# Performance work log

Measured on AMD Instinct MI355X. Metric: run time of the kernel, lower is better.

The kernel has to match this reference:

```python
import jax, jax.numpy as jnp
import numpy as np

WINDOW_LENGTH = 512
ORDER = 26


def hann_window(n):
    # periodic Hann (matches torch.hann_window default)
    i = jnp.arange(n, dtype=jnp.float32)
    return 0.5 * (1.0 - jnp.cos(2.0 * jnp.pi * i / n))


def upsample_linear(g, hop):
    # F.interpolate(mode='linear', align_corners=False), scale_factor=hop
    B, F = g.shape
    j = jnp.arange(F * hop, dtype=jnp.float32)
    src = jnp.clip((j + 0.5) / hop - 0.5, 0.0, F - 1.0)
    i0 = jnp.floor(src).astype(jnp.int32)
    i1 = jnp.minimum(i0 + 1, F - 1)
    w = src - i0.astype(jnp.float32)
    return g[:, i0] * (1.0 - w) + g[:, i1] * w


def lpc_synthesis_batch(x, a):
    # all-pole IIR: y[n] = x[n] - sum_k a[k] * y[n-1-k]; x [N,W], a [N,order]
    N, W = x.shape
    order = a.shape[1]

    def step(carry, xt):  # carry [N,order] newest-first, xt [N]
        yt = xt - jnp.sum(a * carry, axis=1)
        carry = jnp.concatenate([yt[:, None], carry[:, :-1]], axis=1)
        return carry, yt

    _, y = jax.lax.scan(step, jnp.zeros((N, order), x.dtype), x.T)
    return y.T  # [N, W]


def setup_inputs() -> dict:
    key = jax.random.key(0)
    k1, k2, k3 = jax.random.split(key, 3)
    B, T, F = 32, 128000, 1000
    ex = jax.random.normal(k1, (B, T), dtype=jnp.float32)
    gain = jax.random.uniform(k2, (B, F), dtype=jnp.float32)
    # small coefficients keep the all-pole filter stable
    a = jax.random.normal(k3, (B, F, ORDER), dtype=jnp.float32) * 0.05
    window = hann_window(WINDOW_LENGTH)
    return {"ex": ex, "gain": gain, "a": a, "window": window, "hop_length": 128}


def reference(ex, gain, a, window, hop_length):
    W = window.shape[0]
    pad = (W - hop_length) // 2
    B = ex.shape[0]
    ug = upsample_linear(gain, hop_length)  # [B, F*hop]
    T = min(ex.shape[1], ug.shape[1])
    exg = ex[:, :T] * ug[:, :T]
    exp = jnp.pad(exg, ((0, 0), (pad, pad)))
    nframes = (exp.shape[1] - W) // hop_length + 1
    idx = jnp.arange(nframes)[:, None] * hop_length + jnp.arange(W)[None, :]  # [F,W]
    unfolded = exp[:, idx]  # [B, F, W]
    a_ = a[:, :nframes].reshape(-1, a.shape[-1])
    filt = lpc_synthesis_batch(unfolded.reshape(-1, W), a_).reshape(B, nframes, W)
    windowed = filt * window  # window applied per in-frame sample (diag kernel)
    L = (nframes - 1) * hop_length + W
    flat_idx = idx.reshape(-1)
    ola = jnp.zeros((B, L), filt.dtype).at[:, flat_idx].add(windowed.reshape(B, -1))
    norm = jnp.zeros((L,), filt.dtype).at[flat_idx].add(jnp.tile(window, nframes))
    return ola[:, pad:L - pad] / norm[pad:L - pad]
```

## Files before the change

kernel.cpp:

```cpp
#include <hip/hip_runtime.h>
#include <hip/hip_bf16.h>

#define BATCH   32
#define TLEN    128000
#define FGAIN   1000
#define ORDER   26
#define WLEN    512
#define HOP     128
#define PAD     192
#define TPAD    (TLEN + 2*PAD)
#define NFRAME  1000
#define NTOT    (BATCH*NFRAME)

#define CHUNK   64
#define NCHUNK  ((NFRAME + CHUNK - 1) / CHUNK)
#define XS_SPAN (CHUNK*HOP + WLEN - HOP)
#define XS_LDS  8656
#define GS_LDS  80
#define YSTRIDE 53

__global__ __launch_bounds__(64) void k_lpc(const float* __restrict__ ex,
                                            const float* __restrict__ gain,
                                            const float* __restrict__ acoef,
                                            float* __restrict__ fw) {
  __shared__ float xs[XS_LDS];
  __shared__ float gs[GS_LDS];
  __shared__ float ys[CHUNK * YSTRIDE];

  const int lane = threadIdx.x;
  const int n0   = blockIdx.x * CHUNK;
  const int b    = blockIdx.y;
  const float* __restrict__ exr = ex + (size_t)b * TLEN;
  const float* __restrict__ gr  = gain + b * FGAIN;

  const int GBASE = n0 - 2;
  for (int i = lane; i < 72; i += 64) {
    int gidx = GBASE + i;
    gidx = gidx < 0 ? 0 : (gidx > FGAIN - 1 ? FGAIN - 1 : gidx);
    gs[i] = gr[gidx];
  }
  __syncthreads();

  for (int i = lane; i < XS_SPAN / 4; i += 64) {
    int s = 4 * i;
    int j = n0 * HOP + s - PAD;
    float vv[4] = {0.f, 0.f, 0.f, 0.f};
    if (j >= 0 && j < TLEN) {
      float4 e = *reinterpret_cast<const float4*>(exr + j);
      float ee[4] = {e.x, e.y, e.z, e.w};
#pragma unroll
      for (int c = 0; c < 4; ++c) {
        float src = ((float)(j + c) + 0.5f) * (1.0f / (float)HOP) - 0.5f;
        src = fminf(fmaxf(src, 0.0f), (float)(FGAIN - 1));
        int   i0 = (int)src;
        float w  = src - (float)i0;
        int   i1 = i0 + 1; if (i1 > FGAIN - 1) i1 = FGAIN - 1;
        float g  = gs[i0 - GBASE] * (1.0f - w) + gs[i1 - GBASE] * w;
        vv[c] = ee[c] * g;
      }
    }
    int base = s + (s >> 7);
    xs[base + 0] = vv[0];  xs[base + 1] = vv[1];
    xs[base + 2] = vv[2];  xs[base + 3] = vv[3];
  }
  __syncthreads();

  int f = b * NFRAME + n0 + lane;
  int f_cl = f < NTOT ? f : NTOT - 1;
  const float* __restrict__ ap = acoef + (size_t)f_cl * ORDER;
  const size_t fwrow0 = (size_t)(b * NFRAME + n0) * WLEN;

  float a[ORDER], h[ORDER];
#pragma unroll
  for (int q = 0; q < 13; ++q) {
    float2 v = *reinterpret_cast<const float2*>(ap + 2 * q);
    a[2 * q] = v.x;  a[2 * q + 1] = v.y;
  }
#pragma unroll
  for (int k = 0; k < ORDER; ++k) h[k] = 0.0f;

  float buf[52];

#define LPC_STEP(s) {                                                      \
    float xv = buf[(s)];                                                   \
    float p0 = xv, p1 = 0.f, p2 = 0.f, p3 = 0.f;                           \
    _Pragma("unroll")                                                      \
    for (int k = 1; k < ORDER; ++k) {                                      \
      float hv = h[((s) - 1 - k + 2 * ORDER) % ORDER];                     \
      int sel = k & 3;                                                     \
      if      (sel == 0) p0 -= a[k] * hv;                                  \
      else if (sel == 1) p1 -= a[k] * hv;                                  \
      else if (sel == 2) p2 -= a[k] * hv;                                  \
      else               p3 -= a[k] * hv;                                  \
    }                                                                      \
    float rest = (p0 + p1) + (p2 + p3);                                    \
    float y = rest - a[0] * h[((s) + ORDER - 1) % ORDER];                  \
    h[(s) % ORDER] = y;                                                    \
    ys[lane * YSTRIDE + (s)] = y;                                          \
  }

#define LOAD_BUF(nq) {                                                     \
    _Pragma("unroll")                                                      \
    for (int q = 0; q < (nq); ++q) {                                       \
      int u = t + 4 * q;                                                   \
      int base = lane * 129 + u + (u >> 7);                                \
      buf[4 * q + 0] = xs[base + 0];                                       \
      buf[4 * q + 1] = xs[base + 1];                                       \
      buf[4 * q + 2] = xs[base + 2];                                       \
      buf[4 * q + 3] = xs[base + 3];                                       \
    }                                                                      \
  }

#define STORE_YS(nq) {                                                     \
    __syncthreads();                                                       \
    _Pragma("unroll")                                                      \
    for (int jj = 0; jj < 4; ++jj) {                                       \
      int q = (lane & 3) + 4 * jj;                                         \
      if (q < (nq)) {                                                      \
        _Pragma("unroll")                                                  \
        for (int rr = 0; rr < 4; ++rr) {                                   \
          int r = rr * 16 + (lane >> 2);                                   \
          if ((n0 + r) < NFRAME) {                                         \
            float4 vv = make_float4(ys[r * YSTRIDE + 4 * q + 0],           \
                                    ys[r * YSTRIDE + 4 * q + 1],           \
                                    ys[r * YSTRIDE + 4 * q + 2],           \
                                    ys[r * YSTRIDE + 4 * q + 3]);          \
            *reinterpret_cast<float4*>(fw + fwrow0 + (size_t)r * WLEN      \
                                       + t + 4 * q) = vv;                  \
          }                                                                \
        }                                                                  \
      }                                                                    \
    }                                                                      \
    __syncthreads();                                                       \
  }

  int t = 0;
  for (int sb = 0; sb < 9; ++sb) {
    LOAD_BUF(13)
#pragma unroll
    for (int s = 0; s < 52; ++s) {
      LPC_STEP(s)
    }
    STORE_YS(13)
    t += 52;
  }
  LOAD_BUF(11)
#pragma unroll
  for (int s = 0; s < 44; ++s) {
    LPC_STEP(s)
  }
  STORE_YS(11)
#undef LPC_STEP
#undef LOAD_BUF
#undef STORE_YS
}

__global__ __launch_bounds__(256) void k_ola(const float* __restrict__ fw,
                                             const float* __restrict__ win,
                                             float* __restrict__ out) {
  int gid = blockIdx.x * 256 + threadIdx.x;
  const int total4 = BATCH * TLEN / 4;
  if (gid >= total4) return;
  int idx = gid * 4;
  int b  = idx / TLEN;
  int j0 = idx - b * TLEN;
  int p0 = j0 + PAD;

  int lo = (p0 - 381) / HOP;
  if (lo < 0) lo = 0;
  int hi = p0 / HOP;
  if (hi > NFRAME - 1) hi = NFRAME - 1;

  float ax = 0.f, ay = 0.f, az = 0.f, aw = 0.f;
  float nx = 0.f, ny = 0.f, nz = 0.f, nw = 0.f;
  for (int n = lo; n <= hi; ++n) {
    int w0 = p0 - n * HOP;
    const float4 fv = *reinterpret_cast<const float4*>(fw + ((size_t)b * NFRAME + n) * WLEN + w0);
    const float4 wv = *reinterpret_cast<const float4*>(win + w0);
    ax += fv.x * wv.x;  ay += fv.y * wv.y;  az += fv.z * wv.z;  aw += fv.w * wv.w;
    nx += wv.x;         ny += wv.y;         nz += wv.z;         nw += wv.w;
  }
  float4 o = make_float4(ax / nx, ay / ny, az / nz, aw / nw);
  *reinterpret_cast<float4*>(out + idx) = o;
}

extern "C" void kernel_launch(void* const* d_in, const int* in_sizes, int n_in,
                              void* d_out, int out_size, void* d_ws, size_t ws_size,
                              hipStream_t stream) {
  const float* ex   = (const float*)d_in[0];
  const float* gain = (const float*)d_in[1];
  const float* a    = (const float*)d_in[2];
  const float* win  = (const float*)d_in[3];
  float* outp = (float*)d_out;

  float* fw = (float*)d_ws;

  {
    hipLaunchKernelGGL(k_lpc, dim3(NCHUNK, BATCH), dim3(64), 0, stream,
                       ex, gain, a, fw);
  }
  {
    int total4 = BATCH * TLEN / 4;
    int blocks = (total4 + 255) / 256;
    hipLaunchKernelGGL(k_ola, dim3(blocks), dim3(256), 0, stream, fw, win, outp);
  }
}
```

Before: 132.2 us.

## Batch global loads in staging, stage LPC coefs via LDS, use wave-level LDS fences

The excitation staging loop now issues eight float4 global loads before computing gain-interpolated values, so more memory requests are in flight per lane. The LPC coefficients for the chunk are loaded coalesced into LDS and then read per lane, replacing strided per-thread global loads. The __syncthreads around the ys transpose are replaced by s_waitcnt lgkmcnt(0), which is safe only because the block is a single 64-lane wave. The staging bound check changes from j<TLEN to j<=TLEN-4, which holds for these aligned sizes.

```diff
diff --git a/kernel.cpp b/kernel.cpp
--- a/kernel.cpp
+++ b/kernel.cpp
@@ -19,12 +19,15 @@
 #define GS_LDS  80
 #define YSTRIDE 53
 
+#define WAVE_LDS_FENCE() asm volatile("s_waitcnt lgkmcnt(0)" ::: "memory")
+
 __global__ __launch_bounds__(64) void k_lpc(const float* __restrict__ ex,
                                             const float* __restrict__ gain,
                                             const float* __restrict__ acoef,
                                             float* __restrict__ fw) {
   __shared__ float xs[XS_LDS];
   __shared__ float gs[GS_LDS];
+  __shared__ float as_lin[CHUNK * ORDER];
   __shared__ float ys[CHUNK * YSTRIDE];
 
   const int lane = threadIdx.x;
@@ -41,44 +44,88 @@
   }
   __syncthreads();
 
-  for (int i = lane; i < XS_SPAN / 4; i += 64) {
-    int s = 4 * i;
-    int j = n0 * HOP + s - PAD;
-    float vv[4] = {0.f, 0.f, 0.f, 0.f};
-    if (j >= 0 && j < TLEN) {
-      float4 e = *reinterpret_cast<const float4*>(exr + j);
-      float ee[4] = {e.x, e.y, e.z, e.w};
-#pragma unroll
-      for (int c = 0; c < 4; ++c) {
-        float src = ((float)(j + c) + 0.5f) * (1.0f / (float)HOP) - 0.5f;
-        src = fminf(fmaxf(src, 0.0f), (float)(FGAIN - 1));
-        int   i0 = (int)src;
-        float w  = src - (float)i0;
-        int   i1 = i0 + 1; if (i1 > FGAIN - 1) i1 = FGAIN - 1;
-        float g  = gs[i0 - GBASE] * (1.0f - w) + gs[i1 - GBASE] * w;
-        vv[c] = ee[c] * g;
-      }
-    }
-    int base = s + (s >> 7);
-    xs[base + 0] = vv[0];  xs[base + 1] = vv[1];
-    xs[base + 2] = vv[2];  xs[base + 3] = vv[3];
-  }
+  {
+    const int e0_4 = (b * NFRAME + n0) * ORDER / 4;
+    const int lim4 = NTOT * ORDER / 4;
+    for (int v = lane; v < CHUNK * ORDER / 4; v += 64) {
+      float4 c = make_float4(0.f, 0.f, 0.f, 0.f);
+      if (e0_4 + v < lim4)
+        c = *reinterpret_cast<const float4*>(acoef + 4 * (size_t)(e0_4 + v));
+      *reinterpret_cast<float4*>(as_lin + 4 * v) = c;
+    }
+  }
+
+  const int sbase = n0 * HOP;
+#define STAGE_COMPUTE(IDX4, EVAL) {                                        \
+    int sc_s = 4 * (IDX4);                                                 \
+    int sc_j = sbase + sc_s - PAD;                                         \
+    float sc_v[4] = {0.f, 0.f, 0.f, 0.f};                                  \
+    if (sc_j >= 0 && sc_j <= TLEN - 4) {                                   \
+      float sc_e[4] = {(EVAL).x, (EVAL).y, (EVAL).z, (EVAL).w};            \
+      _Pragma("unroll")                                                    \
+      for (int sc_c = 0; sc_c < 4; ++sc_c) {                               \
+        float sc_src = ((float)(sc_j + sc_c) + 0.5f) * (1.0f / (float)HOP) \
+                       - 0.5f;                                             \
+        sc_src = fminf(fmaxf(sc_src, 0.0f), (float)(FGAIN - 1));           \
+        int   sc_i0 = (int)sc_src;                                         \
+        float sc_w  = sc_src - (float)sc_i0;                               \
+        int   sc_i1 = sc_i0 + 1; if (sc_i1 > FGAIN - 1) sc_i1 = FGAIN - 1; \
+        float sc_g  = gs[sc_i0 - GBASE] * (1.0f - sc_w)                    \
+                    + gs[sc_i1 - GBASE] * sc_w;                            \
+        sc_v[sc_c] = sc_e[sc_c] * sc_g;                                    \
+      }                                                                    \
+    }                                                                      \
+    int sc_b = sc_s + (sc_s >> 7);              \
+    xs[sc_b + 0] = sc_v[0];  xs[sc_b + 1] = sc_v[1];                       \
+    xs[sc_b + 2] = sc_v[2];  xs[sc_b + 3] = sc_v[3];                       \
+  }
+  for (int g8 = 0; g8 < 4; ++g8) {
+    float4 ev[8];
+#pragma unroll
+    for (int u = 0; u < 8; ++u) {
+      int gi = lane + 64 * (8 * g8 + u);
+      int gj = sbase + 4 * gi - PAD;
+      ev[u] = make_float4(0.f, 0.f, 0.f, 0.f);
+      if (gj >= 0 && gj <= TLEN - 4)
+        ev[u] = *reinterpret_cast<const float4*>(exr + gj);
+    }
+#pragma unroll
+    for (int u = 0; u < 8; ++u) {
+      STAGE_COMPUTE(lane + 64 * (8 * g8 + u), ev[u])
+    }
+  }
+  {
+    int ti = lane + 2048;
+    int tj = sbase + 4 * ti - PAD;
+    float4 te = make_float4(0.f, 0.f, 0.f, 0.f);
+    if (tj >= 0 && tj <= TLEN - 4)
+      te = *reinterpret_cast<const float4*>(exr + tj);
+    STAGE_COMPUTE(ti, te)
+  }
+  if (lane < XS_SPAN / 4 - 2112) {
+    int ti = lane + 2112;
+    int tj = sbase + 4 * ti - PAD;
+    float4 te = make_float4(0.f, 0.f, 0.f, 0.f);
+    if (tj >= 0 && tj <= TLEN - 4)
+      te = *reinterpret_cast<const float4*>(exr + tj);
+    STAGE_COMPUTE(ti, te)
+  }
+#undef STAGE_COMPUTE
   __syncthreads();
 
-  int f = b * NFRAME + n0 + lane;
-  int f_cl = f < NTOT ? f : NTOT - 1;
-  const float* __restrict__ ap = acoef + (size_t)f_cl * ORDER;
+  float a[ORDER], h[ORDER];
+  {
+    const float* __restrict__ al = as_lin + lane * ORDER;
+#pragma unroll
+    for (int q = 0; q < 13; ++q) {
+      float2 v = *reinterpret_cast<const float2*>(al + 2 * q);
+      a[2 * q] = v.x;  a[2 * q + 1] = v.y;
+    }
+  }
+#pragma unroll
+  for (int k = 0; k < ORDER; ++k) h[k] = 0.0f;
+
   const size_t fwrow0 = (size_t)(b * NFRAME + n0) * WLEN;
-
-  float a[ORDER], h[ORDER];
-#pragma unroll
-  for (int q = 0; q < 13; ++q) {
-    float2 v = *reinterpret_cast<const float2*>(ap + 2 * q);
-    a[2 * q] = v.x;  a[2 * q + 1] = v.y;
-  }
-#pragma unroll
-  for (int k = 0; k < ORDER; ++k) h[k] = 0.0f;
-
   float buf[52];
 
 #define LPC_STEP(s) {                                                      \
@@ -112,7 +159,7 @@
   }
 
 #define STORE_YS(nq) {                                                     \
-    __syncthreads();                                                       \
+    WAVE_LDS_FENCE();          \
     _Pragma("unroll")                                                      \
     for (int jj = 0; jj < 4; ++jj) {                                       \
       int q = (lane & 3) + 4 * jj;                                         \
@@ -131,7 +178,7 @@
         }                                                                  \
       }                                                                    \
     }                                                                      \
-    __syncthreads();                                                       \
+    WAVE_LDS_FENCE();           \
   }
 
   int t = 0;
```

Result: faster. 127.7 us (-3.4%).
